# Kernel tuning notes

Hardware: AMD Instinct MI355X
Metric: run time of the kernel (lower is better)

## Reference

```python
import jax, jax.numpy as jnp
import numpy as np

B, N, NODE_DIM, D, H, K, VP = 64, 1024, 8, 128, 4, 16, 128
FF = 512


def _layernorm(x, g, b):
    m = jnp.mean(x, axis=-1, keepdims=True)
    v = jnp.var(x, axis=-1, keepdims=True)
    return (x - m) * jax.lax.rsqrt(v + 1e-5) * g + b


def setup_inputs() -> dict:
    key = jax.random.key(0)
    kit = iter(jax.random.split(key, 64))

    def w(*shape):
        fan_in = shape[-2] if len(shape) >= 2 else shape[-1]
        return jax.random.normal(next(kit), shape, jnp.float32) / np.sqrt(fan_in)

    return dict(
        node_inputs=jax.random.normal(next(kit), (B, N, NODE_DIM), jnp.float32),
        node_padding_mask=jnp.zeros((B, 1, N), jnp.bool_),
        current_index=jax.random.randint(next(kit), (B, 1, 1), 0, N),
        viewpoints=jax.random.randint(next(kit), (B, VP, 1), 0, N),
        viewpoint_padding_mask=jnp.zeros((B, 1, VP), jnp.bool_),
        adj_list=jax.random.randint(next(kit), (B, N, K), 0, N),
        W_init=w(NODE_DIM, D), b_init=jnp.zeros((D,), jnp.float32),
        gcn_W=w(4, D, D), gcn_b=jnp.zeros((4, D), jnp.float32),
        tc_fc_W=w(D, D), tc_fc_b=jnp.zeros((D,), jnp.float32),
        tc_ln1_g=jnp.ones((D,), jnp.float32), tc_ln1_b=jnp.zeros((D,), jnp.float32),
        Wq=w(D, H * D), bq=jnp.zeros((H * D,), jnp.float32),
        Wk=w(D, H * D), bk=jnp.zeros((H * D,), jnp.float32),
        Wv=w(D, H * D), bv=jnp.zeros((H * D,), jnp.float32),
        tc_ln2_g=jnp.ones((D,), jnp.float32), tc_ln2_b=jnp.zeros((D,), jnp.float32),
        sg_fc_W=w(D, D), sg_fc_b=jnp.zeros((D,), jnp.float32),
        dec_Wq=w(D, D), dec_Wk=w(D, D), dec_Wv=w(D, D), dec_Wo=w(D, D),
        dec_ln1_g=jnp.ones((D,), jnp.float32), dec_ln1_b=jnp.zeros((D,), jnp.float32),
        ff_W1=w(D, FF), ff_b1=jnp.zeros((FF,), jnp.float32),
        ff_W2=w(FF, D), ff_b2=jnp.zeros((D,), jnp.float32),
        dec_ln2_g=jnp.ones((D,), jnp.float32), dec_ln2_b=jnp.zeros((D,), jnp.float32),
        q_W=w(3 * D, 1), q_b=jnp.zeros((1,), jnp.float32),
    )


def _forward(node_inputs, node_padding_mask, current_index, viewpoints, viewpoint_padding_mask, adj_list,
             W_init, b_init, gcn_W, gcn_b, tc_fc_W, tc_fc_b, tc_ln1_g, tc_ln1_b,
             Wq, bq, Wk, bk, Wv, bv, tc_ln2_g, tc_ln2_b, sg_fc_W, sg_fc_b,
             dec_Wq, dec_Wk, dec_Wv, dec_Wo, dec_ln1_g, dec_ln1_b,
             ff_W1, ff_b1, ff_W2, ff_b2, dec_ln2_g, dec_ln2_b, q_W, q_b):
    Bb, Nn, nd = node_inputs.shape
    d = W_init.shape[1]
    nH = Wq.shape[1] // d  # SGFormer attention heads (per-head dim = d)
    BN = Bb * Nn
    # ---- initial embedding + batched block-diagonal sparse edges (prepare_batch_data) ----
    x0 = node_inputs.reshape(BN, nd) @ W_init + b_init
    offset = (jnp.arange(Bb) * Nn)[:, None, None]
    valid = adj_list >= 0
    row = (jnp.broadcast_to(jnp.arange(Nn)[None, :, None], adj_list.shape) + offset).reshape(-1)
    col = (jnp.where(valid, adj_list, 0) + offset).reshape(-1)
    ew = valid.reshape(-1).astype(x0.dtype)
    deg = jax.ops.segment_sum(ew, row, num_segments=BN) + 1.0  # +1 self-loop
    dinv = jax.lax.rsqrt(deg)
    enorm = (dinv[row] * dinv[col] * ew)[:, None]

    def gcn_conv(h, W, b):
        hw = h @ W
        agg = jax.ops.segment_sum(enorm * hw[col], row, num_segments=BN)
        return agg + hw / deg[:, None] + b  # self-loop term D^-1 * x W

    h = x0
    n_layers = gcn_W.shape[0]
    for i in range(n_layers):
        h = gcn_conv(h, gcn_W[i], gcn_b[i])
        if i < n_layers - 1:
            h = jax.nn.relu(h)
    gnn_out = h
    # ---- SGFormer TransConv: fc -> LN -> relu, then linear global attention over all BN nodes ----
    z0 = jax.nn.relu(_layernorm(x0 @ tc_fc_W + tc_fc_b, tc_ln1_g, tc_ln1_b))
    q = (z0 @ Wq + bq).reshape(BN, nH, d)
    k = (z0 @ Wk + bk).reshape(BN, nH, d)
    v = (z0 @ Wv + bv).reshape(BN, nH, d)
    qs = q / jnp.linalg.norm(q)  # global Frobenius norm, as in SGFormer
    ks = k / jnp.linalg.norm(k)
    Nf = jnp.asarray(BN, x0.dtype)
    kvs = jnp.einsum('lhm,lhd->hmd', ks, v)
    num = jnp.einsum('nhm,hmd->nhd', qs, kvs) + Nf * v
    den = jnp.einsum('nhm,hm->nh', qs, ks.sum(axis=0))[..., None] + Nf
    attn = (num / den).mean(axis=1)  # mean over heads -> [BN, d]
    z = jax.nn.relu(_layernorm(0.5 * attn + 0.5 * z0, tc_ln2_g, tc_ln2_b))  # alpha=0.5 residual
    enhanced = ((0.8 * gnn_out + 0.2 * z) @ sg_fc_W + sg_fc_b).reshape(Bb, Nn, d)  # graph_weight=0.8
    # ---- decoder: gather current node, masked cross-attention to all nodes ----
    cur = jnp.take_along_axis(enhanced, jnp.broadcast_to(current_index, (Bb, 1, d)), axis=1)
    dH = 4
    dk = d // dH
    qd = (cur @ dec_Wq).reshape(Bb, 1, dH, dk).transpose(0, 2, 1, 3)
    kd = (enhanced @ dec_Wk).reshape(Bb, Nn, dH, dk).transpose(0, 2, 1, 3)
    vd = (enhanced @ dec_Wv).reshape(Bb, Nn, dH, dk).transpose(0, 2, 1, 3)
    scores = jnp.einsum('bhqe,bhne->bhqn', qd, kd) / np.sqrt(dk).astype(np.float32)
    scores = jnp.where(node_padding_mask[:, None, :, :], -1e9, scores)
    wts = jax.nn.softmax(scores, axis=-1)
    att = jnp.einsum('bhqn,bhne->bhqe', wts, vd).transpose(0, 2, 1, 3).reshape(Bb, 1, d) @ dec_Wo
    t = _layernorm(cur + att, dec_ln1_g, dec_ln1_b)
    glob = _layernorm(t + jax.nn.relu(t @ ff_W1 + ff_b1) @ ff_W2 + ff_b2, dec_ln2_g, dec_ln2_b)
    # ---- Q head: gather viewpoints, concat(global, current, viewpoint) -> Linear(3d, 1) ----
    Vp = viewpoints.shape[1]
    vp = jnp.take_along_axis(enhanced, jnp.broadcast_to(viewpoints, (Bb, Vp, d)), axis=1)
    cs = jnp.concatenate([glob, cur], axis=-1)  # [B,1,2d]
    af = jnp.concatenate([jnp.broadcast_to(cs, (Bb, Vp, 2 * d)), vp], axis=-1)
    return af @ q_W + q_b  # [B, Vp, 1]


def reference(node_inputs, node_padding_mask, current_index, viewpoints, viewpoint_padding_mask, adj_list,
              W_init, b_init, gcn_W, gcn_b, tc_fc_W, tc_fc_b, tc_ln1_g, tc_ln1_b,
              Wq, bq, Wk, bk, Wv, bv, tc_ln2_g, tc_ln2_b, sg_fc_W, sg_fc_b,
              dec_Wq, dec_Wk, dec_Wv, dec_Wo, dec_ln1_g, dec_ln1_b,
              ff_W1, ff_b1, ff_W2, ff_b2, dec_ln2_g, dec_ln2_b, q_W, q_b):
    return _forward(node_inputs, node_padding_mask, current_index, viewpoints, viewpoint_padding_mask, adj_list,
                    W_init, b_init, gcn_W, gcn_b, tc_fc_W, tc_fc_b, tc_ln1_g, tc_ln1_b,
                    Wq, bq, Wk, bk, Wv, bv, tc_ln2_g, tc_ln2_b, sg_fc_W, sg_fc_b,
                    dec_Wq, dec_Wk, dec_Wv, dec_Wo, dec_ln1_g, dec_ln1_b,
                    ff_W1, ff_b1, ff_W2, ff_b2, dec_ln2_g, dec_ln2_b, q_W, q_b)
```

## Files before the change

kernel.cpp:

```cpp
#include <hip/hip_runtime.h>

#define BNn 65536L

typedef unsigned short u16;
typedef unsigned int u32;
typedef __attribute__((ext_vector_type(8))) short short8;
typedef __attribute__((ext_vector_type(4))) float f32x4;

__device__ inline u16 f2b(float f){ u32 u = __float_as_uint(f); u32 r = (u + 0x7fffu + ((u>>16)&1u))>>16; return (u16)r; }
__device__ inline float b2f(u16 b){ return __uint_as_float(((u32)b)<<16); }

__global__ __launch_bounds__(256) void k_init(const float* __restrict__ gcnW, const float* __restrict__ tcW,
                       const float* __restrict__ sgW, const float* __restrict__ dKW,
                       const float* __restrict__ dVW,
                       const float* __restrict__ Wq, const float* __restrict__ Wk, const float* __restrict__ Wv,
                       const float* __restrict__ in, const float* __restrict__ Wi, const float* __restrict__ bi,
                       const int* __restrict__ adj, float* __restrict__ dinv,
                       u16* __restrict__ wts, float* __restrict__ SqSkz, u16* __restrict__ x0) {
  __shared__ u16 sT[64 * 136];
  __shared__ float Ws[1024];
  __shared__ float bs[128];
  __shared__ float ins[256];
  int bid = blockIdx.x, t = threadIdx.x;
  if (bid < 41) {
    if (bid == 40) {
      if (t < 130) SqSkz[t] = 0.0f;
      return;
    }
    const float* src; long dst; int lds_src;
    if (bid < 16) {
      int mtx = bid >> 1, kh = bid & 1;
      src = (mtx < 4 ? gcnW + mtx * 16384 : mtx == 4 ? tcW : mtx == 5 ? sgW : mtx == 6 ? dKW : dVW) + kh * 64 * 128;
      dst = (long)mtx * 16384 + kh * 64;
      lds_src = 128;
    } else {
      int q = bid - 16; int mat = q >> 3, rem = q & 7, kh = rem >> 2, cb = rem & 3;
      src = (mat == 0 ? Wq : mat == 1 ? Wk : Wv) + kh * 64 * 512 + cb * 128;
      dst = 131072L + (long)(mat * 512 + cb * 128) * 128 + kh * 64;
      lds_src = 512;
    }
#pragma unroll
    for (int i = 0; i < 32; i++) {
      int idx = t + i * 256; int row = idx >> 7, col = idx & 127;
      sT[row * 136 + col] = f2b(src[(long)row * lds_src + col]);
    }
    __syncthreads();
    {
      int n = t >> 1, kb = t & 1;
      u16 ob[32];
#pragma unroll
      for (int k = 0; k < 32; k++) ob[k] = sT[(kb * 32 + k) * 136 + n];
      uint4* o4 = (uint4*)(wts + dst + (long)n * 128 + kb * 32);
      uint4* s4 = (uint4*)ob;
#pragma unroll
      for (int k = 0; k < 4; k++) o4[k] = s4[k];
    }
    return;
  }
  int b = bid - 41;
  long row0 = (long)b * 32;
  if (b < 256) {
    int n = b * 256 + t;
    int cnt = 0;
#pragma unroll
    for (int j = 0; j < 16; j++) cnt += (adj[(long)n * 16 + j] >= 0) ? 1 : 0;
    dinv[n] = rsqrtf((float)cnt + 1.0f);
  }
#pragma unroll
  for (int i = 0; i < 4; i++) Ws[t + i * 256] = Wi[t + i * 256];
  if (t < 128) bs[t] = bi[t];
  ins[t] = in[row0 * 8 + t];
  __syncthreads();
  int row = t >> 3, seg = t & 7;
  float acc[16];
#pragma unroll
  for (int i = 0; i < 16; i++) acc[i] = bs[seg * 16 + i];
#pragma unroll
  for (int k = 0; k < 8; k++) {
    float f = ins[row * 8 + k];
#pragma unroll
    for (int i = 0; i < 16; i++) acc[i] += f * Ws[k * 128 + seg * 16 + i];
  }
  u16 ob[16];
#pragma unroll
  for (int i = 0; i < 16; i++) ob[i] = f2b(acc[i]);
  uint4* o4 = (uint4*)(x0 + (row0 + row) * 128 + seg * 16);
  uint4* s4 = (uint4*)ob;
  o4[0] = s4[0]; o4[1] = s4[1];
}

template<int EPI>
__global__ __launch_bounds__(256) void k_gemm(const u16* __restrict__ A,
                                              const u16* __restrict__ WT,
                                              const float* __restrict__ bias,
                                              const float* __restrict__ lng,
                                              const float* __restrict__ lnb,
                                              u16* __restrict__ C,
                                              u16* __restrict__ CT) {
  __shared__ u16 sW[128 * 136];
  int t = threadIdx.x;
  long row0 = (long)blockIdx.x * 128;
  int wave = t >> 6, lane = t & 63, m = lane & 15, g = lane >> 4;
#pragma unroll
  for (int i = 0; i < 8; i++) {
    int idx = t + i * 256; int row = idx >> 4, ch = idx & 15;
    *(float4*)(sW + row * 136 + ch * 8) = *(const float4*)(WT + row * 128 + ch * 8);
  }
  short8 a[2][4];
#pragma unroll
  for (int i = 0; i < 2; i++) {
    const u16* aG = A + (row0 + wave * 32 + i * 16 + m) * 128 + g * 8;
#pragma unroll
    for (int s = 0; s < 4; s++) a[i][s] = *(const short8*)(aG + s * 32);
  }
  __syncthreads();
  f32x4 acc[2][8];
#pragma unroll
  for (int i = 0; i < 2; i++)
#pragma unroll
    for (int c = 0; c < 8; c++) acc[i][c] = (f32x4){0.f, 0.f, 0.f, 0.f};
#pragma unroll
  for (int s = 0; s < 4; s++) {
#pragma unroll
    for (int c = 0; c < 8; c++) {
      short8 bb = *(const short8*)(sW + (c * 16 + m) * 136 + g * 8 + s * 32);
      acc[0][c] = __builtin_amdgcn_mfma_f32_16x16x32_bf16(a[0][s], bb, acc[0][c], 0, 0, 0);
      acc[1][c] = __builtin_amdgcn_mfma_f32_16x16x32_bf16(a[1][s], bb, acc[1][c], 0, 0, 0);
    }
  }
#pragma unroll
  for (int c = 0; c < 8; c++) {
    float bc = bias ? bias[c * 16 + m] : 0.0f;
#pragma unroll
    for (int i = 0; i < 2; i++)
#pragma unroll
      for (int r = 0; r < 4; r++) acc[i][c][r] += bc;
  }
  if (EPI == 2) {
    float gg[8], bb2[8];
#pragma unroll
    for (int c = 0; c < 8; c++) { gg[c] = lng[c * 16 + m]; bb2[c] = lnb[c * 16 + m]; }
#pragma unroll
    for (int i = 0; i < 2; i++)
#pragma unroll
      for (int r = 0; r < 4; r++) {
        float s1 = 0.f, s2 = 0.f;
#pragma unroll
        for (int c = 0; c < 8; c++) { float y = acc[i][c][r]; s1 += y; s2 += y * y; }
#pragma unroll
        for (int mask = 1; mask < 16; mask <<= 1) { s1 += __shfl_xor(s1, mask); s2 += __shfl_xor(s2, mask); }
        float mu = s1 * (1.f / 128.f);
        float rstd = rsqrtf(s2 * (1.f / 128.f) - mu * mu + 1e-5f);
#pragma unroll
        for (int c = 0; c < 8; c++)
          acc[i][c][r] = fmaxf((acc[i][c][r] - mu) * rstd * gg[c] + bb2[c], 0.f);
      }
  }
#pragma unroll
  for (int i = 0; i < 2; i++) {
    long rb = row0 + wave * 32 + i * 16 + g * 4;
#pragma unroll
    for (int c = 0; c < 8; c++) {
      int col = c * 16 + m;
      u16 ob[4];
#pragma unroll
      for (int r = 0; r < 4; r++) {
        float y = acc[i][c][r];
        if (EPI == 1) y = fmaxf(y, 0.f);
        ob[r] = f2b(y);
        C[(rb + r) * 128 + col] = ob[r];
      }
      if (CT) {
        uint2 p;
        p.x = ((u32)ob[1] << 16) | ob[0]; p.y = ((u32)ob[3] << 16) | ob[2];
        *(uint2*)(CT + (long)col * BNn + rb) = p;
      }
    }
  }
}

__global__ __launch_bounds__(256) void k_gcn(const u16* __restrict__ h,
                                             const u16* __restrict__ WT,
                                             const int* __restrict__ adj,
                                             const float* __restrict__ dinv,
                                             const float* __restrict__ gb,
                                             u16* __restrict__ out, int relu) {
  __shared__ u16 sA[64 * 132];
  __shared__ u16 sW[128 * 132];
  int t = threadIdx.x;
  int lane = t & 63;
  int p = blockIdx.x;
  long n0 = ((long)(p & 63) << 10) + ((long)(p >> 6) << 6);
#pragma unroll
  for (int i = 0; i < 8; i++) {
    int idx = t + i * 256; int row = idx >> 4, ch = idx & 15;
    *(float4*)(sW + row * 132 + ch * 8) = *(const float4*)(WT + row * 128 + ch * 8);
  }
  {
    int row = t >> 2, seg = t & 3;
    long n = n0 + row;
    float din = dinv[n];
    float d2v = din * din;
    int4 a4 = *(const int4*)(adj + n * 16 + seg * 4);
    int cols[4]; float enq[4];
    int bb = ((int)(n >> 10)) << 10;
    const int* ap = &a4.x;
#pragma unroll
    for (int q = 0; q < 4; q++) {
      int a = ap[q];
      int valid = a >= 0;
      int cc = (valid ? a : 0) + bb;
      cols[q] = cc;
      enq[q] = valid ? din * dinv[cc] : 0.0f;
    }
    float acc[32];
    {
      const u16* hr = h + n * 128 + seg * 32;
      uint4 v0 = *(const uint4*)(hr), v1 = *(const uint4*)(hr + 8), v2 = *(const uint4*)(hr + 16), v3 = *(const uint4*)(hr + 24);
      const u16* pv = (const u16*)&v0;
#pragma unroll
      for (int i = 0; i < 8; i++) acc[i] = b2f(pv[i]) * d2v;
      pv = (const u16*)&v1;
#pragma unroll
      for (int i = 0; i < 8; i++) acc[8 + i] = b2f(pv[i]) * d2v;
      pv = (const u16*)&v2;
#pragma unroll
      for (int i = 0; i < 8; i++) acc[16 + i] = b2f(pv[i]) * d2v;
      pv = (const u16*)&v3;
#pragma unroll
      for (int i = 0; i < 8; i++) acc[24 + i] = b2f(pv[i]) * d2v;
    }
#pragma unroll
    for (int j = 0; j < 16; j++) {
      int src = (lane & 60) | (j >> 2);
      int cc = __shfl(cols[j & 3], src);
      float e = __shfl(enq[j & 3], src);
      const u16* nb = h + (long)cc * 128 + seg * 32;
      uint4 v0 = *(const uint4*)(nb), v1 = *(const uint4*)(nb + 8), v2 = *(const uint4*)(nb + 16), v3 = *(const uint4*)(nb + 24);
      const u16* pv = (const u16*)&v0;
#pragma unroll
      for (int i = 0; i < 8; i++) acc[i] += e * b2f(pv[i]);
      pv = (const u16*)&v1;
#pragma unroll
      for (int i = 0; i < 8; i++) acc[8 + i] += e * b2f(pv[i]);
      pv = (const u16*)&v2;
#pragma unroll
      for (int i = 0; i < 8; i++) acc[16 + i] += e * b2f(pv[i]);
      pv = (const u16*)&v3;
#pragma unroll
      for (int i = 0; i < 8; i++) acc[24 + i] += e * b2f(pv[i]);
    }
    u16 ob[32];
#pragma unroll
    for (int i = 0; i < 32; i++) ob[i] = f2b(acc[i]);
    uint4* o4 = (uint4*)(sA + row * 132 + seg * 32);
    uint4* s4 = (uint4*)ob;
#pragma unroll
    for (int i = 0; i < 4; i++) o4[i] = s4[i];
  }
  __syncthreads();
  int wave = t >> 6, m = lane & 15, g = lane >> 4;
  const u16* aB = sA + (wave * 16 + m) * 132 + g * 8;
  short8 a[4];
#pragma unroll
  for (int s = 0; s < 4; s++) a[s] = *(const short8*)(aB + s * 32);
  f32x4 acc[8];
#pragma unroll
  for (int c = 0; c < 8; c++) {
    float bc = gb[c * 16 + m];
    acc[c] = (f32x4){bc, bc, bc, bc};
  }
#pragma unroll
  for (int s = 0; s < 4; s++) {
#pragma unroll
    for (int c = 0; c < 8; c++) {
      short8 bb = *(const short8*)(sW + (c * 16 + m) * 132 + g * 8 + s * 32);
      acc[c] = __builtin_amdgcn_mfma_f32_16x16x32_bf16(a[s], bb, acc[c], 0, 0, 0);
    }
  }
#pragma unroll
  for (int c = 0; c < 8; c++) {
    int col = c * 16 + m;
#pragma unroll
    for (int r = 0; r < 4; r++) {
      float y = acc[c][r];
      if (relu) y = fmaxf(y, 0.f);
      out[(n0 + wave * 16 + g * 4 + r) * 128 + col] = f2b(y);
    }
  }
}

__global__ __launch_bounds__(256) void k_gram(const u16* __restrict__ z0T,
                                              float* __restrict__ Gpart, float* __restrict__ zsum) {
  __shared__ u16 sZT[128 * 264];
  int t = threadIdx.x;
  int wave = t >> 6, lane = t & 63, m = lane & 15, g = lane >> 4;
  f32x4 acc[2][8];
#pragma unroll
  for (int i = 0; i < 2; i++)
#pragma unroll
    for (int c = 0; c < 8; c++) acc[i][c] = (f32x4){0.f, 0.f, 0.f, 0.f};
  float zs = 0.f;
  for (int sl = 0; sl < 2; sl++) {
    long k0 = (long)(blockIdx.x * 2 + sl) * 256;
    __syncthreads();
#pragma unroll
    for (int i = 0; i < 16; i++) {
      int idx = t + i * 256; int mm = idx >> 5, ch = idx & 31;
      *(float4*)(sZT + mm * 264 + ch * 8) = *(const float4*)(z0T + (long)mm * BNn + k0 + ch * 8);
    }
    __syncthreads();
#pragma unroll
    for (int kk = 0; kk < 8; kk++) {
      short8 a0 = *(const short8*)(sZT + (wave * 32 + m) * 264 + kk * 32 + g * 8);
      short8 a1 = *(const short8*)(sZT + (wave * 32 + 16 + m) * 264 + kk * 32 + g * 8);
#pragma unroll
      for (int c = 0; c < 8; c++) {
        short8 bb = *(const short8*)(sZT + (c * 16 + m) * 264 + kk * 32 + g * 8);
        acc[0][c] = __builtin_amdgcn_mfma_f32_16x16x32_bf16(a0, bb, acc[0][c], 0, 0, 0);
        acc[1][c] = __builtin_amdgcn_mfma_f32_16x16x32_bf16(a1, bb, acc[1][c], 0, 0, 0);
      }
    }
    if (t < 128) {
      float s = 0.f;
      for (int j = 0; j < 256; j++) s += b2f(sZT[t * 264 + j]);
      zs += s;
    }
  }
  if (t < 128) atomicAdd(&zsum[t], zs);
  float* P = Gpart + (long)blockIdx.x * 16384 + wave * 4096;
#pragma unroll
  for (int i = 0; i < 2; i++)
#pragma unroll
    for (int c = 0; c < 8; c++)
      *(f32x4*)(P + (i * 8 + c) * 256 + lane * 4) = acc[i][c];
}

__global__ void k_gram_red(const float* __restrict__ Gpart, float* __restrict__ G) {
  int o = blockIdx.x * 256 + threadIdx.x;
  float s = 0.f;
  for (int b = 0; b < 128; b++) s += Gpart[(long)b * 16384 + o];
  int wave = o >> 12, rem = o & 4095;
  int ic = rem >> 8, i = ic >> 3, c = ic & 7;
  int rem2 = rem & 255, lane = rem2 >> 2, q = rem2 & 3;
  int m = lane & 15, g = lane >> 4;
  int mi = wave * 32 + i * 16 + g * 4 + q;
  int mj = c * 16 + m;
  G[mi * 128 + mj] = s;
}

__global__ __launch_bounds__(256) void k_statskvs(const float* __restrict__ Wq, const float* __restrict__ bq,
                                                  const float* __restrict__ Wk, const float* __restrict__ bk,
                                                  const float* __restrict__ Wv, const float* __restrict__ bv,
                                                  const float* __restrict__ G, const float* __restrict__ zsum,
                                                  float* __restrict__ ksum,
                                                  float* __restrict__ Sq, float* __restrict__ Sk,
                                                  u16* __restrict__ kvsT) {
  int t = threadIdx.x;
  int blk = blockIdx.x;
  if (blk < 2) {
    int c = blk * 256 + t;
    float s = 0.f;
    for (int i = 0; i < 128; i++) s += Wk[i * 512 + c] * zsum[i];
    ksum[c] = s + 65536.0f * bk[c];
    return;
  }
  if (blk < 130) {
    __shared__ float wcol[128];
    __shared__ float red[256];
    int bi = blk - 2;
    int isK = bi >> 6;
    const float* W = isK ? Wk : Wq;
    const float* bb = isK ? bk : bq;
    float* S = isK ? Sk : Sq;
    int c0 = (bi & 63) * 8;
    float tot = 0.f;
    for (int cc = 0; cc < 8; cc++) {
      int c = c0 + cc;
      __syncthreads();
      if (t < 128) wcol[t] = W[t * 512 + c];
      __syncthreads();
      float v = 0.f;
      if (t < 128) {
        float uu = 0.f;
        for (int j = 0; j < 128; j++) uu += G[t * 128 + j] * wcol[j];
        v = uu * wcol[t] + 2.0f * bb[c] * wcol[t] * zsum[t];
      }
      red[t] = v;
      __syncthreads();
      for (int o = 128; o > 0; o >>= 1) { if (t < o) red[t] += red[t + o]; __syncthreads(); }
      if (t == 0) tot += red[0] + 65536.0f * bb[c] * bb[c];
    }
    if (t == 0) atomicAdd(S, tot);
    return;
  }
  {
    __shared__ float wv8[128][8];
    __shared__ float U[128][8];
    __shared__ float zv[8];
    int bi = blk - 130;
    int h = bi >> 4, dg = bi & 15;
    if (t < 128) {
#pragma unroll
      for (int dd = 0; dd < 8; dd++) wv8[t][dd] = Wv[t * 512 + h * 128 + dg * 8 + dd];
    }
    __syncthreads();
    {
      int i = t & 127, du = t >> 7;
      float a0 = 0.f, a1 = 0.f, a2 = 0.f, a3 = 0.f;
      for (int j = 0; j < 128; j++) {
        float gg = G[i * 128 + j];
        a0 += gg * wv8[j][du * 4 + 0]; a1 += gg * wv8[j][du * 4 + 1];
        a2 += gg * wv8[j][du * 4 + 2]; a3 += gg * wv8[j][du * 4 + 3];
      }
      U[i][du * 4 + 0] = a0; U[i][du * 4 + 1] = a1; U[i][du * 4 + 2] = a2; U[i][du * 4 + 3] = a3;
    }
    if (t < 8) {
      float s = 0.f;
      for (int i = 0; i < 128; i++) s += zsum[i] * wv8[i][t];
      zv[t] = s;
    }
    __syncthreads();
    {
      int m = t & 127, du = t >> 7;
      int colk = h * 128 + m;
      float bkm = bk[colk];
      float a[4] = {0.f, 0.f, 0.f, 0.f};
      float wkzs = 0.f;
      for (int i = 0; i < 128; i++) {
        float wk = Wk[i * 512 + colk];
        wkzs += wk * zsum[i];
#pragma unroll
        for (int q = 0; q < 4; q++) a[q] += wk * U[i][du * 4 + q];
      }
#pragma unroll
      for (int q = 0; q < 4; q++) {
        int dd = du * 4 + q;
        int cold = h * 128 + dg * 8 + dd;
        float val = a[q] + wkzs * bv[cold] + bkm * zv[dd] + 65536.0f * bkm * bv[cold];
        kvsT[h * 16384 + (dg * 8 + dd) * 128 + m] = f2b(val);
      }
    }
  }
}

__global__ __launch_bounds__(256) void k_prepB(const float* __restrict__ Wq, const float* __restrict__ bq,
                                               const float* __restrict__ Wv, const float* __restrict__ bv,
                                               const u16* __restrict__ kvsT, const float* __restrict__ ksum,
                                               const float* __restrict__ SqSk,
                                               u16* __restrict__ Bmat, float* __restrict__ cAv,
                                               u16* __restrict__ U16, float* __restrict__ consts) {
  __shared__ float kvr[8][128];
  int t = threadIdx.x;
  int h = blockIdx.x >> 4, dg = blockIdx.x & 15;
  float inv = rsqrtf(SqSk[0] * SqSk[1]);
  for (int i = t; i < 1024; i += 256) {
    int dl = i >> 7, m = i & 127;
    kvr[dl][m] = b2f(kvsT[h * 16384 + (dg * 8 + dl) * 128 + m]);
  }
  __syncthreads();
  {
    int k = t & 127, du = t >> 7;
    const float* wqr = Wq + k * 512 + h * 128;
    float acc[4] = {0.f, 0.f, 0.f, 0.f};
    for (int m = 0; m < 128; m++) {
      float w = wqr[m];
#pragma unroll
      for (int q = 0; q < 4; q++) acc[q] += w * kvr[du * 4 + q][m];
    }
#pragma unroll
    for (int q = 0; q < 4; q++) {
      int dd = dg * 8 + du * 4 + q;
      float mv = acc[q] * inv + 65536.0f * Wv[k * 512 + h * 128 + dd];
      Bmat[((long)h * 128 + dd) * 128 + k] = f2b(mv);
    }
  }
  if (t < 8) {
    float s = 0.f;
    for (int m = 0; m < 128; m++) s += bq[h * 128 + m] * kvr[t][m];
    cAv[h * 128 + dg * 8 + t] = s * inv + 65536.0f * bv[h * 128 + dg * 8 + t];
  }
  if (dg == 0) {
    if (t < 128) {
      float s = 0.f;
      for (int m = 0; m < 128; m++) s += Wq[t * 512 + h * 128 + m] * ksum[h * 128 + m];
      U16[h * 128 + t] = f2b(s * inv);
    } else if (t == 128) {
      float s = 0.f;
      for (int m = 0; m < 128; m++) s += bq[h * 128 + m] * ksum[h * 128 + m];
      consts[h] = s * inv + 65536.0f;
    }
    if (h == 0) {
      for (int i = t; i < 1536; i += 256) U16[512 + i] = 0;
    }
  }
}

__global__ __launch_bounds__(512) void k_numfuse(const u16* __restrict__ z0, const u16* __restrict__ gnn,
                                                 const u16* __restrict__ Bmat,
                                                 const float* __restrict__ cAv, const u16* __restrict__ U16,
                                                 const float* __restrict__ consts,
                                                 const float* __restrict__ g2, const float* __restrict__ b2,
                                                 const u16* __restrict__ wsg, const float* __restrict__ sgb,
                                                 u16* __restrict__ enh) {
  __shared__ u16 sA[128 * 132];
  __shared__ u16 sB[128 * 132];
  __shared__ float rden[512];
  __shared__ float caL[512];
  int t = threadIdx.x;
  long n0 = (long)blockIdx.x * 128;
  int wave = t >> 6, lane = t & 63, m = lane & 15, g = lane >> 4;
  u16* myA = sA + wave * 16 * 132;
  {
    const u16* zg = z0 + (n0 + wave * 16) * 128;
#pragma unroll
    for (int i = 0; i < 4; i++) {
      int idx = lane + i * 64; int row = idx >> 4, ch = idx & 15;
      *(float4*)(myA + row * 132 + ch * 8) = *(const float4*)(zg + row * 128 + ch * 8);
    }
  }
  caL[t] = cAv[t & 511];
  const u16* aB = sA + (wave * 16 + m) * 132 + g * 8;
  short8 a[4];
#pragma unroll
  for (int s = 0; s < 4; s++) a[s] = *(const short8*)(aB + s * 32);
  {
    f32x4 accd = (f32x4){0.f, 0.f, 0.f, 0.f};
#pragma unroll
    for (int s = 0; s < 4; s++) {
      short8 ub = *(const short8*)(U16 + m * 128 + g * 8 + s * 32);
      accd = __builtin_amdgcn_mfma_f32_16x16x32_bf16(a[s], ub, accd, 0, 0, 0);
    }
    if (m < 4) {
      float ch = consts[m];
#pragma unroll
      for (int r = 0; r < 4; r++)
        rden[(wave * 16 + g * 4 + r) * 4 + m] = 1.0f / (accd[r] + ch);
    }
  }
  f32x4 attn[8];
#pragma unroll
  for (int c = 0; c < 8; c++) attn[c] = (f32x4){0.f, 0.f, 0.f, 0.f};
  for (int h = 0; h < 4; h++) {
    __syncthreads();
    {
      const u16* src = Bmat + (long)h * 16384;
#pragma unroll
      for (int i = 0; i < 4; i++) {
        int idx = t + i * 512; int row = idx >> 4, ch = idx & 15;
        *(float4*)(sB + row * 132 + ch * 8) = *(const float4*)(src + row * 128 + ch * 8);
      }
    }
    __syncthreads();
    f32x4 acc[8];
#pragma unroll
    for (int c = 0; c < 8; c++) {
      float ca = caL[h * 128 + c * 16 + m];
      acc[c] = (f32x4){ca, ca, ca, ca};
    }
#pragma unroll
    for (int s = 0; s < 4; s++) {
#pragma unroll
      for (int c = 0; c < 8; c++) {
        short8 bb = *(const short8*)(sB + (c * 16 + m) * 132 + g * 8 + s * 32);
        acc[c] = __builtin_amdgcn_mfma_f32_16x16x32_bf16(a[s], bb, acc[c], 0, 0, 0);
      }
    }
#pragma unroll
    for (int c = 0; c < 8; c++)
#pragma unroll
      for (int r = 0; r < 4; r++)
        attn[c][r] += acc[c][r] * rden[(wave * 16 + g * 4 + r) * 4 + h];
  }
  float y[8][4];
#pragma unroll
  for (int c = 0; c < 8; c++)
#pragma unroll
    for (int r = 0; r < 4; r++)
      y[c][r] = 0.125f * attn[c][r] + 0.5f * b2f(sA[(wave * 16 + g * 4 + r) * 132 + c * 16 + m]);
  float mu[4], rstd[4];
#pragma unroll
  for (int r = 0; r < 4; r++) {
    float s1 = 0.f, s2 = 0.f;
#pragma unroll
    for (int c = 0; c < 8; c++) { float v = y[c][r]; s1 += v; s2 += v * v; }
#pragma unroll
    for (int mask = 1; mask < 16; mask <<= 1) { s1 += __shfl_xor(s1, mask); s2 += __shfl_xor(s2, mask); }
    float mm2 = s1 * (1.f / 128.f);
    mu[r] = mm2; rstd[r] = rsqrtf(s2 * (1.f / 128.f) - mm2 * mm2 + 1e-5f);
  }
  {
    const u16* gg = gnn + (n0 + wave * 16) * 128;
#pragma unroll
    for (int i = 0; i < 4; i++) {
      int idx = lane + i * 64; int row = idx >> 4, ch = idx & 15;
      *(float4*)(myA + row * 132 + ch * 8) = *(const float4*)(gg + row * 128 + ch * 8);
    }
  }
#pragma unroll
  for (int c = 0; c < 8; c++) {
    int d = c * 16 + m;
    float ggc = g2[d], bbc = b2[d];
#pragma unroll
    for (int r = 0; r < 4; r++) {
      int loc = (wave * 16 + g * 4 + r) * 132 + d;
      float zr = fmaxf((y[c][r] - mu[r]) * rstd[r] * ggc + bbc, 0.f);
      sA[loc] = f2b(0.8f * b2f(sA[loc]) + 0.2f * zr);
    }
  }
  __syncthreads();
  {
#pragma unroll
    for (int i = 0; i < 4; i++) {
      int idx = t + i * 512; int row = idx >> 4, ch = idx & 15;
      *(float4*)(sB + row * 132 + ch * 8) = *(const float4*)(wsg + row * 128 + ch * 8);
    }
  }
  __syncthreads();
  short8 ap[4];
#pragma unroll
  for (int s = 0; s < 4; s++) ap[s] = *(const short8*)(aB + s * 32);
  f32x4 acc2[8];
#pragma unroll
  for (int c = 0; c < 8; c++) {
    float bc = sgb[c * 16 + m];
    acc2[c] = (f32x4){bc, bc, bc, bc};
  }
#pragma unroll
  for (int s = 0; s < 4; s++) {
#pragma unroll
    for (int c = 0; c < 8; c++) {
      short8 bb = *(const short8*)(sB + (c * 16 + m) * 132 + g * 8 + s * 32);
      acc2[c] = __builtin_amdgcn_mfma_f32_16x16x32_bf16(ap[s], bb, acc2[c], 0, 0, 0);
    }
  }
#pragma unroll
  for (int c = 0; c < 8; c++) {
    int d = c * 16 + m;
#pragma unroll
    for (int r = 0; r < 4; r++)
      enh[(n0 + wave * 16 + g * 4 + r) * 128 + d] = f2b(acc2[c][r]);
  }
}

__global__ __launch_bounds__(256) void k_dec(const u16* __restrict__ enh, const int* __restrict__ cidx,
                                             const int* __restrict__ vps,
                                             const float* __restrict__ dWq, const float* __restrict__ dWk,
                                             const float* __restrict__ dWv, const float* __restrict__ dWo,
                                             const float* __restrict__ ln1g, const float* __restrict__ ln1b,
                                             const float* __restrict__ fW1, const float* __restrict__ fb1,
                                             const float* __restrict__ fW2, const float* __restrict__ fb2,
                                             const float* __restrict__ ln2g, const float* __restrict__ ln2b,
                                             const float* __restrict__ qW, const float* __restrict__ qb,
                                             float* __restrict__ out) {
  __shared__ float cur[128], qd[128], qtL[4][128];
  __shared__ float scL[4][1024];
  __shared__ float mxs[4], dinvs[4];
  __shared__ float pvL[4][4][128], sH[4][128];
  __shared__ float att[128], tn[128], tv[128], f1[512], red[256], glob[128];
  __shared__ float mu_s, rs_s, base_s;
  int b = blockIdx.x, t = threadIdx.x;
  int wave = t >> 6, lane = t & 63;
  const u16* eb = enh + (long)b * 1024 * 128;
  if (t < 128) {
    int ci = cidx[b];
    cur[t] = b2f(eb[(long)ci * 128 + t]);
  }
  __syncthreads();
  if (t < 128) {
    float s = 0.f;
    for (int k = 0; k < 128; k++) s += cur[k] * dWq[k * 128 + t];
    qd[t] = s;
  }
  __syncthreads();
  if (t < 128) {
#pragma unroll
    for (int h = 0; h < 4; h++) {
      float s = 0.f;
#pragma unroll
      for (int c = 0; c < 32; c++) s += dWk[t * 128 + h * 32 + c] * qd[h * 32 + c];
      qtL[h][t] = s;
    }
  }
  __syncthreads();
  const float scale = 0.17677669529663687f;
#pragma unroll
  for (int i = 0; i < 4; i++) {
    int n = t * 4 + i;
    const u16* er = eb + (long)n * 128;
    float s0 = 0.f, s1 = 0.f, s2 = 0.f, s3 = 0.f;
#pragma unroll
    for (int i8 = 0; i8 < 16; i8++) {
      short8 ev = *(const short8*)(er + i8 * 8);
#pragma unroll
      for (int j = 0; j < 8; j++) {
        float e = b2f((u16)ev[j]);
        int k = i8 * 8 + j;
        s0 += e * qtL[0][k]; s1 += e * qtL[1][k]; s2 += e * qtL[2][k]; s3 += e * qtL[3][k];
      }
    }
    scL[0][n] = s0 * scale; scL[1][n] = s1 * scale; scL[2][n] = s2 * scale; scL[3][n] = s3 * scale;
  }
  __syncthreads();
  {
    float mx = -3.0e38f;
    for (int k = lane; k < 1024; k += 64) mx = fmaxf(mx, scL[wave][k]);
#pragma unroll
    for (int msk = 1; msk < 64; msk <<= 1) mx = fmaxf(mx, __shfl_xor(mx, msk));
    if (lane == 0) mxs[wave] = mx;
  }
  __syncthreads();
#pragma unroll
  for (int h = 0; h < 4; h++) {
    f32x4 v = *(f32x4*)&scL[h][t * 4];
    float mv = mxs[h];
    v[0] = __expf(v[0] - mv); v[1] = __expf(v[1] - mv); v[2] = __expf(v[2] - mv); v[3] = __expf(v[3] - mv);
    *(f32x4*)&scL[h][t * 4] = v;
  }
  __syncthreads();
  {
    float sm = 0.f;
    for (int k = lane; k < 1024; k += 64) sm += scL[wave][k];
#pragma unroll
    for (int msk = 1; msk < 64; msk <<= 1) sm += __shfl_xor(sm, msk);
    if (lane == 0) dinvs[wave] = 1.0f / sm;
  }
  __syncthreads();
  {
    int seg = t & 15, part = t >> 4;
    float acc[4][8];
#pragma unroll
    for (int h = 0; h < 4; h++)
#pragma unroll
      for (int j = 0; j < 8; j++) acc[h][j] = 0.f;
    for (int i = 0; i < 64; i++) {
      int n = part * 64 + i;
      short8 e8 = *(const short8*)(eb + (long)n * 128 + seg * 8);
      float p0 = scL[0][n], p1 = scL[1][n], p2 = scL[2][n], p3 = scL[3][n];
#pragma unroll
      for (int j = 0; j < 8; j++) {
        float e = b2f((u16)e8[j]);
        acc[0][j] += p0 * e; acc[1][j] += p1 * e; acc[2][j] += p2 * e; acc[3][j] += p3 * e;
      }
    }
#pragma unroll
    for (int h = 0; h < 4; h++)
#pragma unroll
      for (int j = 0; j < 8; j++) {
        acc[h][j] += __shfl_xor(acc[h][j], 16);
        acc[h][j] += __shfl_xor(acc[h][j], 32);
      }
    if (lane < 16) {
#pragma unroll
      for (int h = 0; h < 4; h++)
#pragma unroll
        for (int j = 0; j < 8; j++) pvL[wave][h][seg * 8 + j] = acc[h][j];
    }
  }
  __syncthreads();
  if (t < 128) {
#pragma unroll
    for (int h = 0; h < 4; h++)
      sH[h][t] = pvL[0][h][t] + pvL[1][h][t] + pvL[2][h][t] + pvL[3][h][t];
  }
  __syncthreads();
  if (t < 128) {
    int h = t >> 5, e = t & 31;
    float s = 0.f;
    for (int k = 0; k < 128; k++) s += sH[h][k] * dWv[k * 128 + h * 32 + e];
    att[t] = s * dinvs[h];
  }
  __syncthreads();
  if (t < 128) {
    float s = 0.f;
    for (int k = 0; k < 128; k++) s += att[k] * dWo[k * 128 + t];
    tv[t] = cur[t] + s;
  }
  {
    __syncthreads();
    float v = (t < 128) ? tv[t] : 0.f;
    red[t] = v; __syncthreads();
    for (int o = 128; o > 0; o >>= 1) { if (t < o) red[t] += red[t + o]; __syncthreads(); }
    float s1 = red[0];
    __syncthreads();
    red[t] = v * v; __syncthreads();
    for (int o = 128; o > 0; o >>= 1) { if (t < o) red[t] += red[t + o]; __syncthreads(); }
    if (t == 0) {
      float mm = s1 / 128.0f;
      mu_s = mm; rs_s = rsqrtf(red[0] / 128.0f - mm * mm + 1e-5f);
    }
    __syncthreads();
    if (t < 128) tn[t] = (tv[t] - mu_s) * rs_s * ln1g[t] + ln1b[t];
    __syncthreads();
  }
#pragma unroll
  for (int i = 0; i < 2; i++) {
    int c = t + 256 * i;
    float s = fb1[c];
    for (int k = 0; k < 128; k++) s += tn[k] * fW1[k * 512 + c];
    f1[c] = fmaxf(s, 0.0f);
  }
  __syncthreads();
  if (t < 128) {
    float s = fb2[t];
    for (int k = 0; k < 512; k++) s += f1[k] * fW2[k * 128 + t];
    tv[t] = tn[t] + s;
  }
  {
    __syncthreads();
    float v = (t < 128) ? tv[t] : 0.f;
    red[t] = v; __syncthreads();
    for (int o = 128; o > 0; o >>= 1) { if (t < o) red[t] += red[t + o]; __syncthreads(); }
    float s1 = red[0];
    __syncthreads();
    red[t] = v * v; __syncthreads();
    for (int o = 128; o > 0; o >>= 1) { if (t < o) red[t] += red[t + o]; __syncthreads(); }
    if (t == 0) {
      float mm = s1 / 128.0f;
      mu_s = mm; rs_s = rsqrtf(red[0] / 128.0f - mm * mm + 1e-5f);
    }
    __syncthreads();
    if (t < 128) glob[t] = (tv[t] - mu_s) * rs_s * ln2g[t] + ln2b[t];
    __syncthreads();
  }
  red[t] = (t < 128 ? glob[t] : cur[t - 128]) * qW[t];
  __syncthreads();
  for (int o = 128; o > 0; o >>= 1) { if (t < o) red[t] += red[t + o]; __syncthreads(); }
  if (t == 0) base_s = red[0] + qb[0];
  __syncthreads();
  if (t < 128) {
    int vi = vps[b * 128 + t];
    const u16* er = eb + (long)vi * 128;
    float s = 0.f;
#pragma unroll
    for (int i8 = 0; i8 < 16; i8++) {
      short8 ev = *(const short8*)(er + i8 * 8);
#pragma unroll
      for (int j = 0; j < 8; j++) s += b2f((u16)ev[j]) * qW[256 + i8 * 8 + j];
    }
    out[b * 128 + t] = base_s + s;
  }
}

extern "C" void kernel_launch(void* const* d_in, const int* in_sizes, int n_in,
                              void* d_out, int out_size, void* d_ws, size_t ws_size,
                              hipStream_t stream) {
  const float* node_in = (const float*)d_in[0];
  const int* cur_idx   = (const int*)d_in[2];
  const int* vps       = (const int*)d_in[3];
  const int* adj       = (const int*)d_in[5];
  const float* W_init  = (const float*)d_in[6];
  const float* b_init  = (const float*)d_in[7];
  const float* gcn_W   = (const float*)d_in[8];
  const float* gcn_b   = (const float*)d_in[9];
  const float* tc_fc_W = (const float*)d_in[10];
  const float* tc_fc_b = (const float*)d_in[11];
  const float* ln1g    = (const float*)d_in[12];
  const float* ln1b    = (const float*)d_in[13];
  const float* Wq      = (const float*)d_in[14];
  const float* bq      = (const float*)d_in[15];
  const float* Wk      = (const float*)d_in[16];
  const float* bk      = (const float*)d_in[17];
  const float* Wv      = (const float*)d_in[18];
  const float* bv      = (const float*)d_in[19];
  const float* ln2g    = (const float*)d_in[20];
  const float* ln2b    = (const float*)d_in[21];
  const float* sg_W    = (const float*)d_in[22];
  const float* sg_b    = (const float*)d_in[23];
  const float* dWq     = (const float*)d_in[24];
  const float* dWk     = (const float*)d_in[25];
  const float* dWv     = (const float*)d_in[26];
  const float* dWo     = (const float*)d_in[27];
  const float* dln1g   = (const float*)d_in[28];
  const float* dln1b   = (const float*)d_in[29];
  const float* fW1     = (const float*)d_in[30];
  const float* fb1     = (const float*)d_in[31];
  const float* fW2     = (const float*)d_in[32];
  const float* fb2     = (const float*)d_in[33];
  const float* dln2g   = (const float*)d_in[34];
  const float* dln2b   = (const float*)d_in[35];
  const float* qW      = (const float*)d_in[36];
  const float* qb      = (const float*)d_in[37];

  char* base = (char*)d_ws;
  u16* bufA = (u16*)base;
  u16* bufB = (u16*)(base + 16777216);
  u16* bufC = (u16*)(base + 33554432);
  u16* z0T  = (u16*)(base + 50331648);
  float* Gpart = (float*)(base + 67108864);
  char* sm = base + 83886080;
  u16* kvsT   = (u16*)sm;
  u16* wts    = (u16*)(sm + 131072);
  float* bqkv = (float*)(sm + 131072 + 655360);
  float* ksum = bqkv + 1536;
  float* SqSk = ksum + 512;
  float* zsum = SqSk + 2;
  float* Gm   = zsum + 128;
  float* dinv = Gm + 16384;
  float* cAv  = dinv + BNn;
  float* consts = cAv + 512;
  u16* Bmat = (u16*)(consts + 4);
  u16* U16m = Bmat + 65536;

  k_init<<<2089, 256, 0, stream>>>(gcn_W, tc_fc_W, sg_W, dWk, dWv, Wq, Wk, Wv,
                                   node_in, W_init, b_init, adj, dinv, wts, SqSk, bufA);

  k_gemm<2><<<512, 256, 0, stream>>>(bufA, wts + 4 * 16384, tc_fc_b, ln1g, ln1b, bufB, z0T);

  k_gram<<<128, 256, 0, stream>>>(z0T, Gpart, zsum);
  k_gram_red<<<64, 256, 0, stream>>>(Gpart, Gm);
  k_statskvs<<<194, 256, 0, stream>>>(Wq, bq, Wk, bk, Wv, bv, Gm, zsum, ksum, SqSk, SqSk + 1, kvsT);
  k_prepB<<<64, 256, 0, stream>>>(Wq, bq, Wv, bv, kvsT, ksum, SqSk, Bmat, cAv, U16m, consts);

  k_gcn<<<1024, 256, 0, stream>>>(bufA, wts + 0 * 16384, adj, dinv, gcn_b + 0, bufC, 1);
  k_gcn<<<1024, 256, 0, stream>>>(bufC, wts + 1 * 16384, adj, dinv, gcn_b + 128, bufA, 1);
  k_gcn<<<1024, 256, 0, stream>>>(bufA, wts + 2 * 16384, adj, dinv, gcn_b + 256, bufC, 1);
  k_gcn<<<1024, 256, 0, stream>>>(bufC, wts + 3 * 16384, adj, dinv, gcn_b + 384, bufA, 0);

  k_numfuse<<<512, 512, 0, stream>>>(bufB, bufA, Bmat, cAv, U16m, consts, ln2g, ln2b,
                                     wts + 5 * 16384, sg_b, bufB);

  k_dec<<<64, 256, 0, stream>>>(bufB, cur_idx, vps, dWq, dWk, dWv, dWo, dln1g, dln1b,
                                fW1, fb1, fW2, fb2, dln2g, dln2b, qW, qb, (float*)d_out);
}
```

Baseline: 446.4 us.

## Widen decoder block to 1024 threads with split-K matvecs and shuffle reductions

The decoder kernel now runs 1024 threads per block instead of 256. Each thread scores one node, and the small matrix-vector products are split over 8 threads per output and combined with warp shuffles. The LayerNorm and dot-product tree reductions become wave shuffles plus a tiny shared-memory combine, which removes many barriers. The intent is to shorten the serial latency of this 64-block tail kernel, at the cost of more registers per thread and more shared memory for partial sums.

```diff
diff --git a/kernel.cpp b/kernel.cpp
--- a/kernel.cpp
+++ b/kernel.cpp
@@ -643,7 +643,7 @@
   }
 }
 
-__global__ __launch_bounds__(256) void k_dec(const u16* __restrict__ enh, const int* __restrict__ cidx,
+__global__ __launch_bounds__(1024) void k_dec(const u16* __restrict__ enh, const int* __restrict__ cidx,
                                              const int* __restrict__ vps,
                                              const float* __restrict__ dWq, const float* __restrict__ dWk,
                                              const float* __restrict__ dWv, const float* __restrict__ dWo,
@@ -656,38 +656,37 @@
   __shared__ float cur[128], qd[128], qtL[4][128];
   __shared__ float scL[4][1024];
   __shared__ float mxs[4], dinvs[4];
-  __shared__ float pvL[4][4][128], sH[4][128];
-  __shared__ float att[128], tn[128], tv[128], f1[512], red[256], glob[128];
+  __shared__ float pvL[16][4][128];
+  __shared__ float sH[4][128];
+  __shared__ float att[128], tn[128], tv[128], f1[512], glob[128];
+  __shared__ float red[16], red2[16];
   __shared__ float mu_s, rs_s, base_s;
   int b = blockIdx.x, t = threadIdx.x;
   int wave = t >> 6, lane = t & 63;
   const u16* eb = enh + (long)b * 1024 * 128;
-  if (t < 128) {
-    int ci = cidx[b];
-    cur[t] = b2f(eb[(long)ci * 128 + t]);
-  }
-  __syncthreads();
-  if (t < 128) {
+  if (t < 128) cur[t] = b2f(eb[(long)cidx[b] * 128 + t]);
+  __syncthreads();
+  {
+    int o = t >> 3, p = t & 7;
     float s = 0.f;
-    for (int k = 0; k < 128; k++) s += cur[k] * dWq[k * 128 + t];
-    qd[t] = s;
-  }
-  __syncthreads();
-  if (t < 128) {
-#pragma unroll
-    for (int h = 0; h < 4; h++) {
-      float s = 0.f;
-#pragma unroll
-      for (int c = 0; c < 32; c++) s += dWk[t * 128 + h * 32 + c] * qd[h * 32 + c];
-      qtL[h][t] = s;
-    }
+    int k0 = p * 16;
+#pragma unroll
+    for (int k = 0; k < 16; k++) s += cur[k0 + k] * dWq[(k0 + k) * 128 + o];
+    s += __shfl_xor(s, 1); s += __shfl_xor(s, 2); s += __shfl_xor(s, 4);
+    if (p == 0) qd[o] = s;
+  }
+  __syncthreads();
+  if (t < 512) {
+    int h = t >> 7, col = t & 127;
+    float s = 0.f;
+#pragma unroll
+    for (int c = 0; c < 32; c++) s += dWk[col * 128 + h * 32 + c] * qd[h * 32 + c];
+    qtL[h][col] = s;
   }
   __syncthreads();
   const float scale = 0.17677669529663687f;
-#pragma unroll
-  for (int i = 0; i < 4; i++) {
-    int n = t * 4 + i;
-    const u16* er = eb + (long)n * 128;
+  {
+    const u16* er = eb + (long)t * 128;
     float s0 = 0.f, s1 = 0.f, s2 = 0.f, s3 = 0.f;
 #pragma unroll
     for (int i8 = 0; i8 < 16; i8++) {
@@ -699,10 +698,10 @@
         s0 += e * qtL[0][k]; s1 += e * qtL[1][k]; s2 += e * qtL[2][k]; s3 += e * qtL[3][k];
       }
     }
-    scL[0][n] = s0 * scale; scL[1][n] = s1 * scale; scL[2][n] = s2 * scale; scL[3][n] = s3 * scale;
-  }
-  __syncthreads();
-  {
+    scL[0][t] = s0 * scale; scL[1][t] = s1 * scale; scL[2][t] = s2 * scale; scL[3][t] = s3 * scale;
+  }
+  __syncthreads();
+  if (wave < 4) {
     float mx = -3.0e38f;
     for (int k = lane; k < 1024; k += 64) mx = fmaxf(mx, scL[wave][k]);
 #pragma unroll
@@ -710,15 +709,15 @@
     if (lane == 0) mxs[wave] = mx;
   }
   __syncthreads();
-#pragma unroll
-  for (int h = 0; h < 4; h++) {
-    f32x4 v = *(f32x4*)&scL[h][t * 4];
+  {
+    int h = t >> 8, i4 = (t & 255) * 4;
+    f32x4 v = *(f32x4*)&scL[h][i4];
     float mv = mxs[h];
     v[0] = __expf(v[0] - mv); v[1] = __expf(v[1] - mv); v[2] = __expf(v[2] - mv); v[3] = __expf(v[3] - mv);
-    *(f32x4*)&scL[h][t * 4] = v;
-  }
-  __syncthreads();
-  {
+    *(f32x4*)&scL[h][i4] = v;
+  }
+  __syncthreads();
+  if (wave < 4) {
     float sm = 0.f;
     for (int k = lane; k < 1024; k += 64) sm += scL[wave][k];
 #pragma unroll
@@ -733,8 +732,8 @@
     for (int h = 0; h < 4; h++)
 #pragma unroll
       for (int j = 0; j < 8; j++) acc[h][j] = 0.f;
-    for (int i = 0; i < 64; i++) {
-      int n = part * 64 + i;
+    for (int i = 0; i < 16; i++) {
+      int n = part * 16 + i;
       short8 e8 = *(const short8*)(eb + (long)n * 128 + seg * 8);
       float p0 = scL[0][n], p1 = scL[1][n], p2 = scL[2][n], p3 = scL[3][n];
 #pragma unroll
@@ -758,87 +757,117 @@
     }
   }
   __syncthreads();
-  if (t < 128) {
-#pragma unroll
-    for (int h = 0; h < 4; h++)
-      sH[h][t] = pvL[0][h][t] + pvL[1][h][t] + pvL[2][h][t] + pvL[3][h][t];
-  }
-  __syncthreads();
-  if (t < 128) {
-    int h = t >> 5, e = t & 31;
+  if (t < 512) {
+    int h = t >> 7, d = t & 127;
     float s = 0.f;
-    for (int k = 0; k < 128; k++) s += sH[h][k] * dWv[k * 128 + h * 32 + e];
-    att[t] = s * dinvs[h];
-  }
-  __syncthreads();
-  if (t < 128) {
+#pragma unroll
+    for (int w = 0; w < 16; w++) s += pvL[w][h][d];
+    sH[h][d] = s;
+  }
+  __syncthreads();
+  {
+    int o = t >> 3, p = t & 7;
+    int h = o >> 5, e = o & 31;
     float s = 0.f;
-    for (int k = 0; k < 128; k++) s += att[k] * dWo[k * 128 + t];
-    tv[t] = cur[t] + s;
-  }
-  {
-    __syncthreads();
+    int k0 = p * 16;
+#pragma unroll
+    for (int k = 0; k < 16; k++) s += sH[h][k0 + k] * dWv[(k0 + k) * 128 + h * 32 + e];
+    s += __shfl_xor(s, 1); s += __shfl_xor(s, 2); s += __shfl_xor(s, 4);
+    if (p == 0) att[o] = s * dinvs[h];
+  }
+  __syncthreads();
+  {
+    int o = t >> 3, p = t & 7;
+    float s = 0.f;
+    int k0 = p * 16;
+#pragma unroll
+    for (int k = 0; k < 16; k++) s += att[k0 + k] * dWo[(k0 + k) * 128 + o];
+    s += __shfl_xor(s, 1); s += __shfl_xor(s, 2); s += __shfl_xor(s, 4);
+    if (p == 0) tv[o] = cur[o] + s;
+  }
+  __syncthreads();
+  {
     float v = (t < 128) ? tv[t] : 0.f;
-    red[t] = v; __syncthreads();
-    for (int o = 128; o > 0; o >>= 1) { if (t < o) red[t] += red[t + o]; __syncthreads(); }
-    float s1 = red[0];
-    __syncthreads();
-    red[t] = v * v; __syncthreads();
-    for (int o = 128; o > 0; o >>= 1) { if (t < o) red[t] += red[t + o]; __syncthreads(); }
-    if (t == 0) {
-      float mm = s1 / 128.0f;
-      mu_s = mm; rs_s = rsqrtf(red[0] / 128.0f - mm * mm + 1e-5f);
-    }
-    __syncthreads();
-    if (t < 128) tn[t] = (tv[t] - mu_s) * rs_s * ln1g[t] + ln1b[t];
-    __syncthreads();
-  }
-#pragma unroll
-  for (int i = 0; i < 2; i++) {
-    int c = t + 256 * i;
-    float s = fb1[c];
-    for (int k = 0; k < 128; k++) s += tn[k] * fW1[k * 512 + c];
-    f1[c] = fmaxf(s, 0.0f);
-  }
-  __syncthreads();
-  if (t < 128) {
-    float s = fb2[t];
-    for (int k = 0; k < 512; k++) s += f1[k] * fW2[k * 128 + t];
-    tv[t] = tn[t] + s;
-  }
-  {
-    __syncthreads();
+    float s1 = v, s2 = v * v;
+#pragma unroll
+    for (int msk = 1; msk < 64; msk <<= 1) { s1 += __shfl_xor(s1, msk); s2 += __shfl_xor(s2, msk); }
+    if (lane == 0) { red[wave] = s1; red2[wave] = s2; }
+  }
+  __syncthreads();
+  if (t == 0) {
+    float s1 = 0.f, s2 = 0.f;
+#pragma unroll
+    for (int w = 0; w < 16; w++) { s1 += red[w]; s2 += red2[w]; }
+    float mm = s1 / 128.0f;
+    mu_s = mm; rs_s = rsqrtf(s2 / 128.0f - mm * mm + 1e-5f);
+  }
+  __syncthreads();
+  if (t < 128) tn[t] = (tv[t] - mu_s) * rs_s * ln1g[t] + ln1b[t];
+  __syncthreads();
+  if (t < 512) {
+    float s = fb1[t];
+    for (int k = 0; k < 128; k++) s += tn[k] * fW1[k * 512 + t];
+    f1[t] = fmaxf(s, 0.0f);
+  }
+  __syncthreads();
+  {
+    int o = t >> 3, p = t & 7;
+    float s = 0.f;
+    int k0 = p * 64;
+#pragma unroll
+    for (int k = 0; k < 64; k++) s += f1[k0 + k] * fW2[(k0 + k) * 128 + o];
+    s += __shfl_xor(s, 1); s += __shfl_xor(s, 2); s += __shfl_xor(s, 4);
+    if (p == 0) tv[o] = tn[o] + s + fb2[o];
+  }
+  __syncthreads();
+  {
     float v = (t < 128) ? tv[t] : 0.f;
-    red[t] = v; __syncthreads();
-    for (int o = 128; o > 0; o >>= 1) { if (t < o) red[t] += red[t + o]; __syncthreads(); }
-    float s1 = red[0];
-    __syncthreads();
-    red[t] = v * v; __syncthreads();
-    for (int o = 128; o > 0; o >>= 1) { if (t < o) red[t] += red[t + o]; __syncthreads(); }
-    if (t == 0) {
-      float mm = s1 / 128.0f;
-      mu_s = mm; rs_s = rsqrtf(red[0] / 128.0f - mm * mm + 1e-5f);
-    }
-    __syncthreads();
-    if (t < 128) glob[t] = (tv[t] - mu_s) * rs_s * ln2g[t] + ln2b[t];
-    __syncthreads();
-  }
-  red[t] = (t < 128 ? glob[t] : cur[t - 128]) * qW[t];
-  __syncthreads();
-  for (int o = 128; o > 0; o >>= 1) { if (t < o) red[t] += red[t + o]; __syncthreads(); }
-  if (t == 0) base_s = red[0] + qb[0];
-  __syncthreads();
-  if (t < 128) {
-    int vi = vps[b * 128 + t];
-    const u16* er = eb + (long)vi * 128;
+    float s1 = v, s2 = v * v;
+#pragma unroll
+    for (int msk = 1; msk < 64; msk <<= 1) { s1 += __shfl_xor(s1, msk); s2 += __shfl_xor(s2, msk); }
+    if (lane == 0) { red[wave] = s1; red2[wave] = s2; }
+  }
+  __syncthreads();
+  if (t == 0) {
+    float s1 = 0.f, s2 = 0.f;
+#pragma unroll
+    for (int w = 0; w < 16; w++) { s1 += red[w]; s2 += red2[w]; }
+    float mm = s1 / 128.0f;
+    mu_s = mm; rs_s = rsqrtf(s2 / 128.0f - mm * mm + 1e-5f);
+  }
+  __syncthreads();
+  if (t < 128) glob[t] = (tv[t] - mu_s) * rs_s * ln2g[t] + ln2b[t];
+  __syncthreads();
+  {
+    float v = 0.f;
+    if (t < 256) v = (t < 128 ? glob[t] : cur[t - 128]) * qW[t];
+    float s = v;
+#pragma unroll
+    for (int msk = 1; msk < 64; msk <<= 1) s += __shfl_xor(s, msk);
+    if (lane == 0) red[wave] = s;
+  }
+  __syncthreads();
+  if (t == 0) {
     float s = 0.f;
 #pragma unroll
-    for (int i8 = 0; i8 < 16; i8++) {
-      short8 ev = *(const short8*)(er + i8 * 8);
-#pragma unroll
-      for (int j = 0; j < 8; j++) s += b2f((u16)ev[j]) * qW[256 + i8 * 8 + j];
-    }
-    out[b * 128 + t] = base_s + s;
+    for (int w = 0; w < 16; w++) s += red[w];
+    base_s = s + qb[0];
+  }
+  __syncthreads();
+  {
+    int o = t >> 3, p = t & 7;
+    int vi = vps[b * 128 + o];
+    const u16* er = eb + (long)vi * 128 + p * 16;
+    short8 e0 = *(const short8*)(er);
+    short8 e1 = *(const short8*)(er + 8);
+    float s = 0.f;
+#pragma unroll
+    for (int j = 0; j < 8; j++) {
+      s += b2f((u16)e0[j]) * qW[256 + p * 16 + j];
+      s += b2f((u16)e1[j]) * qW[256 + p * 16 + 8 + j];
+    }
+    s += __shfl_xor(s, 1); s += __shfl_xor(s, 2); s += __shfl_xor(s, 4);
+    if (p == 0) out[b * 128 + o] = base_s + s;
   }
 }
 
@@ -920,6 +949,6 @@
   k_numfuse<<<512, 512, 0, stream>>>(bufB, bufA, Bmat, cAv, U16m, consts, ln2g, ln2b,
                                      wts + 5 * 16384, sg_b, bufB);
 
-  k_dec<<<64, 256, 0, stream>>>(bufB, cur_idx, vps, dWq, dWk, dWv, dWo, dln1g, dln1b,
-                                fW1, fb1, fW2, fb2, dln2g, dln2b, qW, qb, (float*)d_out);
+  k_dec<<<64, 1024, 0, stream>>>(bufB, cur_idx, vps, dWq, dWk, dWv, dWo, dln1g, dln1b,
+                                 fW1, fb1, fW2, fb2, dln2g, dln2b, qW, qb, (float*)d_out);
 }
```

Measured after the change: 444.1 us. About the same (-0.5%).
